# Optimization experiments

Measured on AMD Instinct MI355X. Metric: run time of the kernel, lower is better.

Reference implementation:

```python
import jax, jax.numpy as jnp
import numpy as np

B, D, C = 512, 512, 100000
M1, M2, M3 = 1.0, 0.5, 0.0  # canonical ArcFace margins
EPS = 1e-12  # tf.nn.l2_normalize epsilon


def _l2norm(v, axis):
    return v * jax.lax.rsqrt(jnp.maximum(jnp.sum(v * v, axis=axis, keepdims=True), EPS))


def setup_inputs() -> dict:
    key = jax.random.key(0)
    k1, k2, k3 = jax.random.split(key, 3)
    x = jax.random.normal(k1, (B, D), dtype=jnp.float32)
    W = jax.random.normal(k2, (D, C), dtype=jnp.float32)
    label_idx = jax.random.randint(k3, (B,), 0, C, dtype=jnp.int32)
    return {"x": x, "W": W, "label_idx": label_idx}


def reference(x, W, label_idx):
    xn = _l2norm(x, axis=1)            # [B, D] unit embeddings
    Wn = _l2norm(W, axis=0)            # [D, C] unit class weights (norm=True fc)
    logits = xn @ Wn                   # [B, C] cosine similarities
    # gather target cosine per row (gather_nd over one-hot label)
    t = jnp.take_along_axis(logits, label_idx[:, None], axis=1)[:, 0]  # [B]
    # m1 == 1.0 -> skip angular scaling branch; m2 != 0 -> additive angular margin
    t = jnp.arccos(t) + M2
    # clamp to pi value-wise, straight-through gradient: t1 = t + pi - stop_grad(t)
    t = jnp.minimum(t, t + (jnp.pi - jax.lax.stop_gradient(t)))
    t = jnp.cos(t)
    onehot = jax.nn.one_hot(label_idx, C, dtype=logits.dtype)  # [B, C]
    out = logits * (1.0 - onehot) + t[:, None] * onehot
    out = out - onehot * M3
    return out
```

## Files before the change

kernel.cpp:

```cpp
#include <hip/hip_runtime.h>
#include <math.h>

#define BB 512
#define DD 512
#define CC 100000
#define MARGIN2 0.5f
#define PI_F 3.14159265358979323846f

#define BM 128
#define BN 128
#define BK 64
#define KSTEPS (DD / BK)
#define NPAN 782
#define GRID (4 * NPAN)

typedef __bf16 bf16x8 __attribute__((ext_vector_type(8)));
typedef float f32x4 __attribute__((ext_vector_type(4)));

static __device__ __forceinline__ unsigned short f2bf(float f) {
    union { float f; unsigned u; } v; v.f = f;
    unsigned r = v.u + 0x7FFFu + ((v.u >> 16) & 1u);
    return (unsigned short)(r >> 16);
}

static __device__ __forceinline__ int swz(int row, int kbyte) {
    return row * 128 + (kbyte ^ ((row & 7) << 4));
}

static __device__ __forceinline__ void gll16(const unsigned char* g, unsigned char* l) {
    __builtin_amdgcn_global_load_lds(
        (const __attribute__((address_space(1))) void*)g,
        (__attribute__((address_space(3))) void*)l, 16, 0, 0);
}

__global__ __launch_bounds__(256) void k_norm_x(const float* __restrict__ x,
                                                unsigned char* __restrict__ img) {
    const int lane = threadIdx.x & 63;
    const int row  = blockIdx.x * 4 + (threadIdx.x >> 6);
    const float* xr = x + (size_t)row * DD;
    float4 v0 = *(const float4*)(xr + lane * 4);
    float4 v1 = *(const float4*)(xr + lane * 4 + 256);
    float s = v0.x*v0.x + v0.y*v0.y + v0.z*v0.z + v0.w*v0.w
            + v1.x*v1.x + v1.y*v1.y + v1.z*v1.z + v1.w*v1.w;
    #pragma unroll
    for (int m = 32; m; m >>= 1) s += __shfl_xor(s, m, 64);
    float rs = rsqrtf(fmaxf(s, 1e-12f));
    ushort4 o0, o1;
    o0.x = f2bf(v0.x * rs); o0.y = f2bf(v0.y * rs);
    o0.z = f2bf(v0.z * rs); o0.w = f2bf(v0.w * rs);
    o1.x = f2bf(v1.x * rs); o1.y = f2bf(v1.y * rs);
    o1.z = f2bf(v1.z * rs); o1.w = f2bf(v1.w * rs);

    const int mb   = row >> 7;
    const int lrow = row & 127;
    const int k0   = lane * 4;
    const int t0   = k0 >> 6;
    const int c8   = (k0 >> 3) & 7;
    const int sub  = (k0 >> 2) & 1;
    const int base = (mb * 8 + t0) * 16384 + lrow * 128
                   + ((c8 * 16) ^ ((lrow & 7) << 4)) + sub * 8;
    *(ushort4*)(img + base)         = o0;
    *(ushort4*)(img + base + 65536) = o1;
}

#define ABUF 16384
#define LDSZ (2 * ABUF + 2 * 16384 + 512)

__global__ __launch_bounds__(256, 2) void k_gemm(const unsigned char* __restrict__ img,
                                                 const float* __restrict__ W,
                                                 float* __restrict__ out) {
    __shared__ __align__(16) unsigned char LDS[LDSZ];
    unsigned char* bufA = LDS;
    unsigned char* bufB = LDS + 2 * ABUF;
    float* rn = (float*)(LDS + 2 * ABUF + 32768);

    const int tid = threadIdx.x;
    const int bid = blockIdx.x;

    const int v  = (bid & 7) * 391 + (bid >> 3);
    const int mb = v & 3;
    const int nb = v >> 2;
    const int M0 = mb * BM;
    const int N0 = nb * BN;

    const int lane = tid & 63;
    const int wid  = tid >> 6;
    const int wm = wid >> 1;
    const int wn = wid & 1;
    const int lr = lane & 15;
    const int lg = lane >> 4;

    int b_go[8], b_ld[8];
    #pragma unroll
    for (int i = 0; i < 8; ++i) {
        int s  = tid + i * 256;
        int n  = s & 127;
        int kq = s >> 7;
        int col = N0 + n;
        col = col < CC ? col : CC - 1;
        b_go[i] = kq * 4 * CC + col;
        b_ld[i] = n * 128 + ((kq * 8) ^ ((n & 7) << 4));
    }

    const unsigned char* imgA = img + mb * (8 * ABUF);
    const int lds_u = wid * 4096;

    float    f0[8][4], f1[8][4];
    unsigned pk[16];
    float    bsq[8] = {0.f, 0.f, 0.f, 0.f, 0.f, 0.f, 0.f, 0.f};

#define WAITV_(N) asm volatile("s_waitcnt vmcnt(" #N ")" ::: "memory")
#define WAITV(N) WAITV_(N)
#define SB() __builtin_amdgcn_sched_barrier(0)

#define LOAD_B(FR, T) do {                                                     \
    _Pragma("unroll")                                                          \
    for (int i = 0; i < 8; ++i) {                                              \
        const float* p = W + b_go[i] + (size_t)(T) * (BK * CC);                \
        FR[i][0] = p[0];      FR[i][1] = p[CC];                                \
        FR[i][2] = p[2 * CC]; FR[i][3] = p[3 * CC];                            \
    } } while (0)

#define PACK(FR) do {                                                          \
    _Pragma("unroll")                                                          \
    for (int i = 0; i < 8; ++i) {                                              \
        bsq[i] += FR[i][0] * FR[i][0] + FR[i][1] * FR[i][1]                    \
                + FR[i][2] * FR[i][2] + FR[i][3] * FR[i][3];                   \
        asm("v_cvt_pk_bf16_f32 %0, %1, %2" : "=v"(pk[2*i])   : "v"(FR[i][0]), "v"(FR[i][1])); \
        asm("v_cvt_pk_bf16_f32 %0, %1, %2" : "=v"(pk[2*i+1]) : "v"(FR[i][2]), "v"(FR[i][3])); \
    } } while (0)

#define WRITE_PK(T) do {                                                       \
    unsigned char* dst = bufB + ((T) & 1) * 16384;                             \
    _Pragma("unroll")                                                          \
    for (int i = 0; i < 8; ++i) {                                              \
        uint2 w; w.x = pk[2*i]; w.y = pk[2*i+1];                               \
        *(uint2*)(dst + b_ld[i]) = w;                                          \
    } } while (0)

#define GLL_A(T) do {                                                          \
    unsigned char* A_nxt = bufA + ((T) & 1) * ABUF;                            \
    const unsigned char* gsrc = imgA + (T) * ABUF;                             \
    _Pragma("unroll")                                                          \
    for (int i = 0; i < 4; ++i)                                                \
        gll16(gsrc + lds_u + i * 1024 + lane * 16, A_nxt + lds_u + i * 1024);  \
    } while (0)

#define COMPUTE(T) do {                                                        \
    const unsigned char* A_cur = bufA + ((T) & 1) * ABUF;                      \
    const unsigned char* B_cur = bufB + ((T) & 1) * 16384;                     \
    __builtin_amdgcn_s_setprio(1);                                             \
    _Pragma("unroll")                                                          \
    for (int ks = 0; ks < 2; ++ks) {                                           \
        bf16x8 af[4];                                                          \
        _Pragma("unroll")                                                      \
        for (int mf = 0; mf < 4; ++mf)                                         \
            af[mf] = *(const bf16x8*)(A_cur + swz(wm * 64 + mf * 16 + lr, ks * 64 + lg * 16)); \
        _Pragma("unroll")                                                      \
        for (int nf = 0; nf < 4; ++nf) {                                       \
            bf16x8 bfr = *(const bf16x8*)(B_cur + swz(wn * 64 + nf * 16 + lr, ks * 64 + lg * 16)); \
            _Pragma("unroll")                                                  \
            for (int mf = 0; mf < 4; ++mf)                                     \
                acc[mf][nf] = __builtin_amdgcn_mfma_f32_16x16x32_bf16(         \
                    bfr, af[mf], acc[mf][nf], 0, 0, 0);                        \
        }                                                                      \
    }                                                                          \
    __builtin_amdgcn_s_setprio(0);                                             \
    } while (0)

#define KBODY(T, FP, FN) do {                                                  \
    if ((T) + 1 < KSTEPS) GLL_A((T) + 1);                                      \
    SB();                                                                      \
    COMPUTE(T);                                                                \
    SB();                                                                      \
    if ((T) + 1 < KSTEPS) { PACK(FP); WRITE_PK((T) + 1); }                     \
    if ((T) + 2 < KSTEPS) LOAD_B(FN, (T) + 2);                                 \
    SB();                                                                      \
    if ((T) + 1 < KSTEPS) {                                                    \
        if ((T) + 2 < KSTEPS) { WAITV(32); } else { WAITV(0); }                \
        SB();                                                                  \
        asm volatile("s_waitcnt lgkmcnt(0)" ::: "memory"); SB();               \
        __builtin_amdgcn_s_barrier(); SB();                                    \
    } } while (0)

    f32x4 acc[4][4];
    #pragma unroll
    for (int mf = 0; mf < 4; ++mf)
        #pragma unroll
        for (int nf = 0; nf < 4; ++nf)
            acc[mf][nf] = (f32x4)0.f;

    LOAD_B(f0, 0);
    GLL_A(0);
    SB();
    PACK(f0); WRITE_PK(0);
    LOAD_B(f1, 1);
    SB();
    WAITV(32); SB();
    asm volatile("s_waitcnt lgkmcnt(0)" ::: "memory"); SB();
    __builtin_amdgcn_s_barrier(); SB();

    KBODY(0, f1, f0);
    KBODY(1, f0, f1);
    KBODY(2, f1, f0);
    KBODY(3, f0, f1);
    KBODY(4, f1, f0);
    KBODY(5, f0, f1);
    KBODY(6, f1, f0);
    KBODY(7, f0, f1);

    __syncthreads();
    float* part = (float*)bufB;
    #pragma unroll
    for (int i = 0; i < 8; ++i)
        part[tid + i * 256] = bsq[i];
    __syncthreads();
    if (tid < BN) {
        float s = 0.f;
        #pragma unroll
        for (int k = 0; k < 16; ++k)
            s += part[k * BN + tid];
        rn[tid] = rsqrtf(fmaxf(s, 1e-12f));
    }
    __syncthreads();

    float* stag = (float*)bufA;
    #pragma unroll
    for (int rd = 0; rd < 4; ++rd) {
        if (wm == (rd >> 1)) {
            #pragma unroll
            for (int f = 0; f < 2; ++f) {
                const int mf = (rd & 1) * 2 + f;
                const int ml = f * 16 + lr;
                #pragma unroll
                for (int nf = 0; nf < 4; ++nf) {
                    const int nl = wn * 64 + nf * 16 + lg * 4;
                    const f32x4 rn4 = *(const f32x4*)(rn + nl);
                    f32x4 o;
                    #pragma unroll
                    for (int r = 0; r < 4; ++r)
                        o[r] = acc[mf][nf][r] * rn4[r];
                    *(f32x4*)(stag + ml * 132 + nl) = o;
                }
            }
        }
        __syncthreads();
        #pragma unroll
        for (int j = tid; j < 1024; j += 256) {
            const int m = j >> 5;
            const int n = (j & 31) * 4;
            if (N0 + n + 4 <= CC) {
                f32x4 o = *(const f32x4*)(stag + m * 132 + n);
                __builtin_nontemporal_store(o,
                    (f32x4*)(out + (size_t)(M0 + rd * 32 + m) * CC + N0 + n));
            }
        }
        __syncthreads();
    }
}

__global__ __launch_bounds__(512) void k_fix(const int* __restrict__ lab,
                                             float* __restrict__ out) {
    const int b = threadIdx.x;
    const int c = lab[b];
    const size_t idx = (size_t)b * CC + c;
    float t = out[idx];
    t = fminf(fmaxf(t, -1.f), 1.f);
    float th = acosf(t) + MARGIN2;
    th = fminf(th, PI_F);
    out[idx] = cosf(th);
}

extern "C" void kernel_launch(void* const* d_in, const int* in_sizes, int n_in,
                              void* d_out, int out_size, void* d_ws, size_t ws_size,
                              hipStream_t stream) {
    const float* x   = (const float*)d_in[0];
    const float* W   = (const float*)d_in[1];
    const int*   lab = (const int*)d_in[2];
    float* out = (float*)d_out;

    unsigned char* img = (unsigned char*)d_ws;

    k_norm_x<<<dim3(BB / 4), dim3(256), 0, stream>>>(x, img);
    k_gemm<<<dim3(GRID), dim3(256), 0, stream>>>(img, W, out);
    k_fix<<<dim3(1), dim3(512), 0, stream>>>(lab, out);
}
```

Before: 121.9 us.

## Use 512-thread blocks with 2x4 wave layout to raise occupancy in GEMM

Doubles the GEMM block from 256 to 512 threads. Waves now form a 2x4 grid, each computing a 64x32 sub-tile instead of 64x64, and the per-thread W loads, packing and A async copies are halved to match. Packing and LDS writes are fused so fewer registers stay live, aiming for more resident waves (launch bounds 512,4) to hide the latency of the strided fp32 W loads. In exchange each wave does less MFMA work per LDS fragment read, adds barrier participants, and the A fragments are now reloaded by more waves.

```diff
diff --git a/kernel.cpp b/kernel.cpp
--- a/kernel.cpp
+++ b/kernel.cpp
@@ -66,7 +66,7 @@
 #define ABUF 16384
 #define LDSZ (2 * ABUF + 2 * 16384 + 512)
 
-__global__ __launch_bounds__(256, 2) void k_gemm(const unsigned char* __restrict__ img,
+__global__ __launch_bounds__(512, 4) void k_gemm(const unsigned char* __restrict__ img,
                                                  const float* __restrict__ W,
                                                  float* __restrict__ out) {
     __shared__ __align__(16) unsigned char LDS[LDSZ];
@@ -85,15 +85,15 @@
 
     const int lane = tid & 63;
     const int wid  = tid >> 6;
-    const int wm = wid >> 1;
-    const int wn = wid & 1;
+    const int wm = wid >> 2;
+    const int wn = wid & 3;
     const int lr = lane & 15;
     const int lg = lane >> 4;
 
-    int b_go[8], b_ld[8];
-    #pragma unroll
-    for (int i = 0; i < 8; ++i) {
-        int s  = tid + i * 256;
+    int b_go[4], b_ld[4];
+    #pragma unroll
+    for (int i = 0; i < 4; ++i) {
+        int s  = tid + i * 512;
         int n  = s & 127;
         int kq = s >> 7;
         int col = N0 + n;
@@ -103,11 +103,10 @@
     }
 
     const unsigned char* imgA = img + mb * (8 * ABUF);
-    const int lds_u = wid * 4096;
-
-    float    f0[8][4], f1[8][4];
-    unsigned pk[16];
-    float    bsq[8] = {0.f, 0.f, 0.f, 0.f, 0.f, 0.f, 0.f, 0.f};
+    const int lds_u = wid * 2048;
+
+    float f0[4][4], f1[4][4];
+    float bsq[4] = {0.f, 0.f, 0.f, 0.f};
 
 #define WAITV_(N) asm volatile("s_waitcnt vmcnt(" #N ")" ::: "memory")
 #define WAITV(N) WAITV_(N)
@@ -115,35 +114,30 @@
 
 #define LOAD_B(FR, T) do {                                                     \
     _Pragma("unroll")                                                          \
-    for (int i = 0; i < 8; ++i) {                                              \
+    for (int i = 0; i < 4; ++i) {                                              \
         const float* p = W + b_go[i] + (size_t)(T) * (BK * CC);                \
         FR[i][0] = p[0];      FR[i][1] = p[CC];                                \
         FR[i][2] = p[2 * CC]; FR[i][3] = p[3 * CC];                            \
     } } while (0)
 
-#define PACK(FR) do {                                                          \
+#define PACK_WRITE(FR, T) do {                                                 \
+    unsigned char* dst = bufB + ((T) & 1) * 16384;                             \
     _Pragma("unroll")                                                          \
-    for (int i = 0; i < 8; ++i) {                                              \
+    for (int i = 0; i < 4; ++i) {                                              \
         bsq[i] += FR[i][0] * FR[i][0] + FR[i][1] * FR[i][1]                    \
                 + FR[i][2] * FR[i][2] + FR[i][3] * FR[i][3];                   \
-        asm("v_cvt_pk_bf16_f32 %0, %1, %2" : "=v"(pk[2*i])   : "v"(FR[i][0]), "v"(FR[i][1])); \
-        asm("v_cvt_pk_bf16_f32 %0, %1, %2" : "=v"(pk[2*i+1]) : "v"(FR[i][2]), "v"(FR[i][3])); \
-    } } while (0)
-
-#define WRITE_PK(T) do {                                                       \
-    unsigned char* dst = bufB + ((T) & 1) * 16384;                             \
-    _Pragma("unroll")                                                          \
-    for (int i = 0; i < 8; ++i) {                                              \
-        uint2 w; w.x = pk[2*i]; w.y = pk[2*i+1];                               \
+        unsigned w0, w1;                                                       \
+        asm("v_cvt_pk_bf16_f32 %0, %1, %2" : "=v"(w0) : "v"(FR[i][0]), "v"(FR[i][1])); \
+        asm("v_cvt_pk_bf16_f32 %0, %1, %2" : "=v"(w1) : "v"(FR[i][2]), "v"(FR[i][3])); \
+        uint2 w; w.x = w0; w.y = w1;                                           \
         *(uint2*)(dst + b_ld[i]) = w;                                          \
     } } while (0)
 
 #define GLL_A(T) do {                                                          \
     unsigned char* A_nxt = bufA + ((T) & 1) * ABUF;                            \
     const unsigned char* gsrc = imgA + (T) * ABUF;                             \
-    _Pragma("unroll")                                                          \
-    for (int i = 0; i < 4; ++i)                                                \
-        gll16(gsrc + lds_u + i * 1024 + lane * 16, A_nxt + lds_u + i * 1024);  \
+    gll16(gsrc + lds_u + lane * 16, A_nxt + lds_u);                            \
+    gll16(gsrc + lds_u + 1024 + lane * 16, A_nxt + lds_u + 1024);              \
     } while (0)
 
 #define COMPUTE(T) do {                                                        \
@@ -152,18 +146,19 @@
     __builtin_amdgcn_s_setprio(1);                                             \
     _Pragma("unroll")                                                          \
     for (int ks = 0; ks < 2; ++ks) {                                           \
-        bf16x8 af[4];                                                          \
+        bf16x8 af[4], bfr[2];                                                  \
         _Pragma("unroll")                                                      \
         for (int mf = 0; mf < 4; ++mf)                                         \
             af[mf] = *(const bf16x8*)(A_cur + swz(wm * 64 + mf * 16 + lr, ks * 64 + lg * 16)); \
         _Pragma("unroll")                                                      \
-        for (int nf = 0; nf < 4; ++nf) {                                       \
-            bf16x8 bfr = *(const bf16x8*)(B_cur + swz(wn * 64 + nf * 16 + lr, ks * 64 + lg * 16)); \
+        for (int nf = 0; nf < 2; ++nf)                                         \
+            bfr[nf] = *(const bf16x8*)(B_cur + swz(wn * 32 + nf * 16 + lr, ks * 64 + lg * 16)); \
+        _Pragma("unroll")                                                      \
+        for (int mf = 0; mf < 4; ++mf)                                         \
             _Pragma("unroll")                                                  \
-            for (int mf = 0; mf < 4; ++mf)                                     \
+            for (int nf = 0; nf < 2; ++nf)                                     \
                 acc[mf][nf] = __builtin_amdgcn_mfma_f32_16x16x32_bf16(         \
-                    bfr, af[mf], acc[mf][nf], 0, 0, 0);                        \
-        }                                                                      \
+                    bfr[nf], af[mf], acc[mf][nf], 0, 0, 0);                    \
     }                                                                          \
     __builtin_amdgcn_s_setprio(0);                                             \
     } while (0)
@@ -173,30 +168,30 @@
     SB();                                                                      \
     COMPUTE(T);                                                                \
     SB();                                                                      \
-    if ((T) + 1 < KSTEPS) { PACK(FP); WRITE_PK((T) + 1); }                     \
+    if ((T) + 1 < KSTEPS) PACK_WRITE(FP, (T) + 1);                             \
     if ((T) + 2 < KSTEPS) LOAD_B(FN, (T) + 2);                                 \
     SB();                                                                      \
     if ((T) + 1 < KSTEPS) {                                                    \
-        if ((T) + 2 < KSTEPS) { WAITV(32); } else { WAITV(0); }                \
+        if ((T) + 2 < KSTEPS) { WAITV(16); } else { WAITV(0); }                \
         SB();                                                                  \
         asm volatile("s_waitcnt lgkmcnt(0)" ::: "memory"); SB();               \
         __builtin_amdgcn_s_barrier(); SB();                                    \
     } } while (0)
 
-    f32x4 acc[4][4];
+    f32x4 acc[4][2];
     #pragma unroll
     for (int mf = 0; mf < 4; ++mf)
         #pragma unroll
-        for (int nf = 0; nf < 4; ++nf)
+        for (int nf = 0; nf < 2; ++nf)
             acc[mf][nf] = (f32x4)0.f;
 
     LOAD_B(f0, 0);
     GLL_A(0);
     SB();
-    PACK(f0); WRITE_PK(0);
+    PACK_WRITE(f0, 0);
     LOAD_B(f1, 1);
     SB();
-    WAITV(32); SB();
+    WAITV(16); SB();
     asm volatile("s_waitcnt lgkmcnt(0)" ::: "memory"); SB();
     __builtin_amdgcn_s_barrier(); SB();
 
@@ -212,8 +207,8 @@
     __syncthreads();
     float* part = (float*)bufB;
     #pragma unroll
-    for (int i = 0; i < 8; ++i)
-        part[tid + i * 256] = bsq[i];
+    for (int i = 0; i < 4; ++i)
+        part[tid + i * 512] = bsq[i];
     __syncthreads();
     if (tid < BN) {
         float s = 0.f;
@@ -233,8 +228,8 @@
                 const int mf = (rd & 1) * 2 + f;
                 const int ml = f * 16 + lr;
                 #pragma unroll
-                for (int nf = 0; nf < 4; ++nf) {
-                    const int nl = wn * 64 + nf * 16 + lg * 4;
+                for (int nf = 0; nf < 2; ++nf) {
+                    const int nl = wn * 32 + nf * 16 + lg * 4;
                     const f32x4 rn4 = *(const f32x4*)(rn + nl);
                     f32x4 o;
                     #pragma unroll
@@ -246,7 +241,7 @@
         }
         __syncthreads();
         #pragma unroll
-        for (int j = tid; j < 1024; j += 256) {
+        for (int j = tid; j < 1024; j += 512) {
             const int m = j >> 5;
             const int n = (j & 31) * 4;
             if (N0 + n + 4 <= CC) {
@@ -282,6 +277,6 @@
     unsigned char* img = (unsigned char*)d_ws;
 
     k_norm_x<<<dim3(BB / 4), dim3(256), 0, stream>>>(x, img);
-    k_gemm<<<dim3(GRID), dim3(256), 0, stream>>>(img, W, out);
+    k_gemm<<<dim3(GRID), dim3(512), 0, stream>>>(img, W, out);
     k_fix<<<dim3(1), dim3(512), 0, stream>>>(lab, out);
 }
```

Result: faster. 110.3 us (-9.5%).
